# Performance work log

Hardware: AMD Instinct MI355X
Metric: run time of the kernel (lower is better)

The kernel has to match this reference:

```python
import jax, jax.numpy as jnp
import numpy as np

S, B, D, H, F, E = 2048, 8, 512, 8, 2048, 64
CAP_FACTOR = 2
EPS = 1e-5


def setup_inputs() -> dict:
    key = jax.random.key(0)
    ks = jax.random.split(key, 12)
    s = 0.02
    return {
        "src": jax.random.normal(ks[0], (S, B, D), jnp.float32),
        "in_proj_w": jax.random.normal(ks[1], (3 * D, D), jnp.float32) * s,
        "in_proj_b": jnp.zeros((3 * D,), jnp.float32),
        "out_proj_w": jax.random.normal(ks[2], (D, D), jnp.float32) * s,
        "out_proj_b": jnp.zeros((D,), jnp.float32),
        "ln1_g": jnp.ones((D,), jnp.float32),
        "ln1_b": jnp.zeros((D,), jnp.float32),
        "gate_w": jax.random.normal(ks[3], (D, E), jnp.float32) * s,
        "w1": jax.random.normal(ks[4], (E, D, F), jnp.float32) * s,
        "b1": jnp.zeros((E, F), jnp.float32),
        "w2": jax.random.normal(ks[5], (E, F, D), jnp.float32) * s,
        "b2": jnp.zeros((E, D), jnp.float32),
        "ln2_g": jnp.ones((D,), jnp.float32),
        "ln2_b": jnp.zeros((D,), jnp.float32),
    }


def _layer_norm(x, g, b):
    mu = jnp.mean(x, -1, keepdims=True)
    var = jnp.mean(jnp.square(x - mu), -1, keepdims=True)
    return (x - mu) * jax.lax.rsqrt(var + EPS) * g + b


def reference(src, in_proj_w, in_proj_b, out_proj_w, out_proj_b,
              ln1_g, ln1_b, gate_w, w1, b1, w2, b2, ln2_g, ln2_b):
    hd = D // H
    # --- self attention (seq-first, as nn.MultiheadAttention) ---
    qkv = src @ in_proj_w.T + in_proj_b            # [S,B,3D]
    q, k, v = jnp.split(qkv, 3, axis=-1)
    q = q.reshape(S, B, H, hd)
    k = k.reshape(S, B, H, hd)
    v = v.reshape(S, B, H, hd)
    scores = jnp.einsum('qbhd,kbhd->bhqk', q, k) * (hd ** -0.5)
    attn = jax.nn.softmax(scores, axis=-1)
    ctx = jnp.einsum('bhqk,kbhd->qbhd', attn, v).reshape(S, B, D)
    attn_out = ctx @ out_proj_w.T + out_proj_b
    x = _layer_norm(src + attn_out, ln1_g, ln1_b)

    # --- MoE: top-1 gating + capacity dispatch + merged expert FFN ---
    N = S * B
    C = CAP_FACTOR * N // E                         # per-expert capacity
    xt = x.reshape(N, D)
    probs = jax.nn.softmax(xt @ gate_w, axis=-1)    # [N,E]
    eidx = jnp.argmax(probs, axis=-1)               # [N]
    gval = jnp.take_along_axis(probs, eidx[:, None], 1)[:, 0]
    onehot = jax.nn.one_hot(eidx, E, dtype=jnp.int32)
    pos = jnp.take_along_axis(jnp.cumsum(onehot, 0), eidx[:, None], 1)[:, 0] - 1
    pos_s = jnp.where(pos < C, pos, C)              # overflow tokens -> dummy slot C
    buf = jnp.zeros((E, C + 1, D), xt.dtype).at[eidx, pos_s].set(xt)
    xe = buf[:, :C]                                 # [E,C,D]
    h = jax.nn.relu(jnp.einsum('ecd,edf->ecf', xe, w1) + b1[:, None, :])
    ye = jnp.einsum('ecf,efd->ecd', h, w2) + b2[:, None, :]
    ye = jnp.pad(ye, ((0, 0), (0, 1), (0, 0)))      # slot C = zeros (dropped)
    yt = ye[eidx, pos_s] * gval[:, None]            # combine with gate weight
    moe_out = yt.reshape(S, B, D)

    return _layer_norm(x + moe_out, ln2_g, ln2_b)
```

## Files before the change

### kernel.cpp

```cpp
#include <hip/hip_runtime.h>
#include <hip/hip_bf16.h>

typedef __bf16 bf16_t;
typedef __bf16 bf16x8 __attribute__((ext_vector_type(8)));
typedef float f32x4 __attribute__((ext_vector_type(4)));

static constexpr int S_ = 2048;
static constexpr int B_ = 8;
static constexpr int D_ = 512;
static constexpr int H_ = 8;
static constexpr int HD_ = 64;
static constexpr int F_ = 2048;
static constexpr int E_ = 64;
static constexpr int NT = S_ * B_;
static constexpr int CAP = 512;
static constexpr float EPS_ = 1e-5f;

__device__ __forceinline__ float wave_sum(float v) {
#pragma unroll
  for (int m = 1; m < 64; m <<= 1) v += __shfl_xor(v, m);
  return v;
}

__global__ void k_cvt(const float* __restrict__ in, bf16_t* __restrict__ out, int n8) {
  int i = blockIdx.x * blockDim.x + threadIdx.x;
  if (i >= n8) return;
  const float4* p = (const float4*)in + (size_t)i * 2;
  float4 a = p[0], b = p[1];
  bf16x8 o;
  o[0]=(bf16_t)a.x; o[1]=(bf16_t)a.y; o[2]=(bf16_t)a.z; o[3]=(bf16_t)a.w;
  o[4]=(bf16_t)b.x; o[5]=(bf16_t)b.y; o[6]=(bf16_t)b.z; o[7]=(bf16_t)b.w;
  ((bf16x8*)out)[i] = o;
}

__global__ void k_tcvt(const float* __restrict__ in, bf16_t* __restrict__ out,
                       int R, int C, long strideIn, long strideOut) {
  __shared__ __align__(16) float t[64][68];
  const float* ip = in + (long)blockIdx.z * strideIn;
  bf16_t* op = out + (long)blockIdx.z * strideOut;
  int r0 = blockIdx.y * 64, c0 = blockIdx.x * 64;
  int tid = threadIdx.x;
  int row = tid >> 2, cc = (tid & 3) * 16;
  const float4* g = (const float4*)(ip + (long)(r0 + row) * C + c0 + cc);
  float4 a0 = g[0], a1 = g[1], a2 = g[2], a3 = g[3];
  *(float4*)&t[row][cc + 0]  = a0;
  *(float4*)&t[row][cc + 4]  = a1;
  *(float4*)&t[row][cc + 8]  = a2;
  *(float4*)&t[row][cc + 12] = a3;
  __syncthreads();
  int oc = tid >> 2, rr = (tid & 3) * 16;
  bf16x8 o0, o1;
#pragma unroll
  for (int j = 0; j < 8; j++) o0[j] = (bf16_t)t[rr + j][oc];
#pragma unroll
  for (int j = 0; j < 8; j++) o1[j] = (bf16_t)t[rr + 8 + j][oc];
  *(bf16x8*)(op + (long)(c0 + oc) * R + r0 + rr)     = o0;
  *(bf16x8*)(op + (long)(c0 + oc) * R + r0 + rr + 8) = o1;
}

__global__ void k_tv(const bf16_t* __restrict__ qkv, bf16_t* __restrict__ vT) {
  __shared__ __align__(16) bf16_t t[64][72];
  int bh = blockIdx.y, bI = bh >> 3, hI = bh & 7;
  int s0 = blockIdx.x * 64;
  int tid = threadIdx.x;
  int row = tid >> 2, cc = (tid & 3) * 16;
  const uint4* g = (const uint4*)(qkv + ((long)(s0 + row) * B_ + bI) * 1536 + 1024 + hI * 64 + cc);
  uint4 v0 = g[0], v1 = g[1];
  *(uint4*)&t[row][cc]     = v0;
  *(uint4*)&t[row][cc + 8] = v1;
  __syncthreads();
  int oc = tid >> 2, rr = (tid & 3) * 16;
  bf16x8 o0, o1;
#pragma unroll
  for (int j = 0; j < 8; j++) o0[j] = t[rr + j][oc];
#pragma unroll
  for (int j = 0; j < 8; j++) o1[j] = t[rr + 8 + j][oc];
  bf16_t* op = vT + ((long)bh * 64 + oc) * (long)S_ + s0 + rr;
  *(bf16x8*)(op)     = o0;
  *(bf16x8*)(op + 8) = o1;
}

template <int RELU>
__global__ __launch_bounds__(256) void k_gemm(
    const bf16_t* __restrict__ A, const bf16_t* __restrict__ Bm,
    const float* __restrict__ bias, bf16_t* __restrict__ Cout,
    int K, int lda, int ldb, int ldc,
    long aStride, long bStride, long cStride, int biasStride,
    const int* __restrict__ cnt, int mCap) {
  __shared__ __align__(16) bf16_t As[128 * 32];
  __shared__ __align__(16) bf16_t Bs[128 * 32];
  int z = blockIdx.z;
  if (cnt) {
    int c = cnt[z]; if (c > mCap) c = mCap;
    if ((int)blockIdx.y * 128 >= c) return;
  }
  long m0 = (long)blockIdx.y * 128, n0 = (long)blockIdx.x * 128;
  const bf16_t* Ab = A + (long)z * aStride + m0 * lda;
  const bf16_t* Bb = Bm + (long)z * bStride + n0 * ldb;
  int tid = threadIdx.x, wid = tid >> 6, lane = tid & 63;
  int lr = lane & 15, lg = lane >> 4;
  int wm = wid >> 1, wn = wid & 1;
  int srow = tid >> 1, scol = (tid & 1) * 16;
  f32x4 acc[4][4] = {};
  const uint4* ga = (const uint4*)(Ab + (long)srow * lda + scol);
  const uint4* gb = (const uint4*)(Bb + (long)srow * ldb + scol);
  uint4 ra0 = ga[0], ra1 = ga[1], rb0 = gb[0], rb1 = gb[1];
  for (int k0 = 0; k0 < K; k0 += 32) {
    *(uint4*)&As[srow * 32 + scol]     = ra0;
    *(uint4*)&As[srow * 32 + scol + 8] = ra1;
    *(uint4*)&Bs[srow * 32 + scol]     = rb0;
    *(uint4*)&Bs[srow * 32 + scol + 8] = rb1;
    __syncthreads();
    if (k0 + 32 < K) {
      ga = (const uint4*)(Ab + (long)srow * lda + (k0 + 32) + scol);
      gb = (const uint4*)(Bb + (long)srow * ldb + (k0 + 32) + scol);
      ra0 = ga[0]; ra1 = ga[1]; rb0 = gb[0]; rb1 = gb[1];
    }
    bf16x8 af[4], bfr[4];
#pragma unroll
    for (int i = 0; i < 4; i++) {
      af[i]  = *(const bf16x8*)&As[(wm * 64 + i * 16 + lr) * 32 + lg * 8];
      bfr[i] = *(const bf16x8*)&Bs[(wn * 64 + i * 16 + lr) * 32 + lg * 8];
    }
#pragma unroll
    for (int i = 0; i < 4; i++)
#pragma unroll
      for (int j = 0; j < 4; j++)
        acc[i][j] = __builtin_amdgcn_mfma_f32_16x16x32_bf16(af[i], bfr[j], acc[i][j], 0, 0, 0);
    __syncthreads();
  }
#pragma unroll
  for (int j = 0; j < 4; j++) {
    int col = (int)n0 + wn * 64 + j * 16 + lr;
    float bv = bias[(long)z * biasStride + col];
#pragma unroll
    for (int i = 0; i < 4; i++) {
      long row = m0 + wm * 64 + i * 16 + lg * 4;
#pragma unroll
      for (int r = 0; r < 4; r++) {
        float v = acc[i][j][r] + bv;
        if (RELU) v = fmaxf(v, 0.0f);
        Cout[(long)z * cStride + (row + r) * ldc + col] = (bf16_t)v;
      }
    }
  }
}

__global__ __launch_bounds__(256) void k_attn(const bf16_t* __restrict__ qkv,
                                              const bf16_t* __restrict__ vT,
                                              bf16_t* __restrict__ ctx) {
  constexpr int LP = 80;
  __shared__ __align__(16) bf16_t Kld[64 * LP];
  __shared__ __align__(16) bf16_t Vld[64 * LP];
  __shared__ __align__(16) bf16_t Pld[4][16 * LP];
  int bh = blockIdx.y, bI = bh >> 3, hI = bh & 7;
  int q0 = blockIdx.x * 64;
  int tid = threadIdx.x, wid = tid >> 6, lane = tid & 63;
  int lr = lane & 15, lg = lane >> 4;
  int qrow = q0 + wid * 16 + lr;
  const bf16_t* qb = qkv + ((long)qrow * B_ + bI) * 1536 + hI * 64;
  bf16x8 qf0 = *(const bf16x8*)(qb + lg * 8);
  bf16x8 qf1 = *(const bf16x8*)(qb + 32 + lg * 8);
  f32x4 o[4] = {};
  float mrun[4], lrun[4];
#pragma unroll
  for (int r = 0; r < 4; r++) { mrun[r] = -3.0e38f; lrun[r] = 0.0f; }
  int srow = tid >> 2, sc = (tid & 3) * 16;
  for (int kb = 0; kb < S_ / 64; kb++) {
    int krow = kb * 64 + srow;
    const uint4* kg = (const uint4*)(qkv + ((long)krow * B_ + bI) * 1536 + 512 + hI * 64 + sc);
    const uint4* vg = (const uint4*)(vT + ((long)bh * 64 + srow) * (long)S_ + kb * 64 + sc);
    uint4 k0v = kg[0], k1v = kg[1], v0v = vg[0], v1v = vg[1];
    __syncthreads();
    *(uint4*)&Kld[srow * LP + sc]     = k0v;
    *(uint4*)&Kld[srow * LP + sc + 8] = k1v;
    *(uint4*)&Vld[srow * LP + sc]     = v0v;
    *(uint4*)&Vld[srow * LP + sc + 8] = v1v;
    __syncthreads();
    f32x4 sacc[4] = {};
#pragma unroll
    for (int kc = 0; kc < 2; kc++) {
      bf16x8 qf = kc ? qf1 : qf0;
#pragma unroll
      for (int kt = 0; kt < 4; kt++) {
        bf16x8 kf = *(const bf16x8*)&Kld[(kt * 16 + lr) * LP + kc * 32 + lg * 8];
        sacc[kt] = __builtin_amdgcn_mfma_f32_16x16x32_bf16(qf, kf, sacc[kt], 0, 0, 0);
      }
    }
#pragma unroll
    for (int kt = 0; kt < 4; kt++) sacc[kt] *= 0.125f;
    float pv[4][4];
#pragma unroll
    for (int r = 0; r < 4; r++) {
      float mx = fmaxf(fmaxf(sacc[0][r], sacc[1][r]), fmaxf(sacc[2][r], sacc[3][r]));
      mx = fmaxf(mx, __shfl_xor(mx, 1));
      mx = fmaxf(mx, __shfl_xor(mx, 2));
      mx = fmaxf(mx, __shfl_xor(mx, 4));
      mx = fmaxf(mx, __shfl_xor(mx, 8));
      float mnew = fmaxf(mrun[r], mx);
      float corr = __expf(mrun[r] - mnew);
      float ps = 0.0f;
#pragma unroll
      for (int kt = 0; kt < 4; kt++) {
        float p = __expf(sacc[kt][r] - mnew);
        pv[kt][r] = p; ps += p;
      }
      ps += __shfl_xor(ps, 1); ps += __shfl_xor(ps, 2);
      ps += __shfl_xor(ps, 4); ps += __shfl_xor(ps, 8);
      lrun[r] = lrun[r] * corr + ps;
      mrun[r] = mnew;
#pragma unroll
      for (int nt = 0; nt < 4; nt++) o[nt][r] *= corr;
    }
#pragma unroll
    for (int kt = 0; kt < 4; kt++)
#pragma unroll
      for (int r = 0; r < 4; r++)
        Pld[wid][(lg * 4 + r) * LP + kt * 16 + lr] = (bf16_t)pv[kt][r];
#pragma unroll
    for (int ks = 0; ks < 2; ks++) {
      bf16x8 pa = *(const bf16x8*)&Pld[wid][lr * LP + ks * 32 + lg * 8];
#pragma unroll
      for (int nt = 0; nt < 4; nt++) {
        bf16x8 vb = *(const bf16x8*)&Vld[(nt * 16 + lr) * LP + ks * 32 + lg * 8];
        o[nt] = __builtin_amdgcn_mfma_f32_16x16x32_bf16(pa, vb, o[nt], 0, 0, 0);
      }
    }
  }
#pragma unroll
  for (int nt = 0; nt < 4; nt++)
#pragma unroll
    for (int r = 0; r < 4; r++) {
      int qr = q0 + wid * 16 + lg * 4 + r;
      float val = o[nt][r] / lrun[r];
      ctx[((long)qr * B_ + bI) * (long)D_ + hI * 64 + nt * 16 + lr] = (bf16_t)val;
    }
}

__global__ void k_ln_res(const float* __restrict__ base, const bf16_t* __restrict__ addb,
                         const float* __restrict__ g, const float* __restrict__ b,
                         float* __restrict__ out) {
  int w = (int)((blockIdx.x * blockDim.x + threadIdx.x) >> 6);
  int lane = threadIdx.x & 63;
  if (w >= NT) return;
  long off = (long)w * D_ + lane * 8;
  const float4* pb = (const float4*)(base + off);
  float4 b0 = pb[0], b1 = pb[1];
  bf16x8 av = *(const bf16x8*)(addb + off);
  float t[8];
  t[0]=b0.x+(float)av[0]; t[1]=b0.y+(float)av[1]; t[2]=b0.z+(float)av[2]; t[3]=b0.w+(float)av[3];
  t[4]=b1.x+(float)av[4]; t[5]=b1.y+(float)av[5]; t[6]=b1.z+(float)av[6]; t[7]=b1.w+(float)av[7];
  float s = t[0]+t[1]+t[2]+t[3]+t[4]+t[5]+t[6]+t[7];
  s = wave_sum(s);
  float mu = s * (1.0f / D_);
  float vv = 0.0f;
#pragma unroll
  for (int j = 0; j < 8; j++) { float d = t[j] - mu; vv += d * d; }
  vv = wave_sum(vv);
  float rstd = rsqrtf(vv * (1.0f / D_) + EPS_);
  const float4* pg = (const float4*)(g + lane * 8);
  const float4* pq = (const float4*)(b + lane * 8);
  float4 g0 = pg[0], g1 = pg[1], q0 = pq[0], q1 = pq[1];
  float4 o0, o1;
  o0.x=(t[0]-mu)*rstd*g0.x+q0.x; o0.y=(t[1]-mu)*rstd*g0.y+q0.y;
  o0.z=(t[2]-mu)*rstd*g0.z+q0.z; o0.w=(t[3]-mu)*rstd*g0.w+q0.w;
  o1.x=(t[4]-mu)*rstd*g1.x+q1.x; o1.y=(t[5]-mu)*rstd*g1.y+q1.y;
  o1.z=(t[6]-mu)*rstd*g1.z+q1.z; o1.w=(t[7]-mu)*rstd*g1.w+q1.w;
  float4* po = (float4*)(out + off);
  po[0] = o0; po[1] = o1;
}

__global__ void k_gate(const float* __restrict__ x, const float* __restrict__ gw,
                       int* __restrict__ eidx, float* __restrict__ gval) {
  int w = (int)((blockIdx.x * blockDim.x + threadIdx.x) >> 6);
  int lane = threadIdx.x & 63;
  if (w >= NT) return;
  const float* xr = x + (long)w * D_;
  float a0 = 0.0f, a1 = 0.0f, a2 = 0.0f, a3 = 0.0f;
#pragma unroll 4
  for (int k = 0; k < D_; k += 4) {
    a0 = fmaf(xr[k + 0], gw[(k + 0) * E_ + lane], a0);
    a1 = fmaf(xr[k + 1], gw[(k + 1) * E_ + lane], a1);
    a2 = fmaf(xr[k + 2], gw[(k + 2) * E_ + lane], a2);
    a3 = fmaf(xr[k + 3], gw[(k + 3) * E_ + lane], a3);
  }
  float acc = (a0 + a1) + (a2 + a3);
  float v = acc; int idx = lane;
#pragma unroll
  for (int m = 1; m < 64; m <<= 1) {
    float ov = __shfl_xor(v, m);
    int oi = __shfl_xor(idx, m);
    if (ov > v || (ov == v && oi < idx)) { v = ov; idx = oi; }
  }
  float s = __expf(acc - v);
  s = wave_sum(s);
  if (lane == 0) { eidx[w] = idx; gval[w] = 1.0f / s; }
}

__global__ void k_route(const float* __restrict__ x, const int* __restrict__ eidx,
                        int* __restrict__ pos, int* __restrict__ cnt,
                        bf16_t* __restrict__ xe) {
  int w = (int)((blockIdx.x * blockDim.x + threadIdx.x) >> 6);
  int lane = threadIdx.x & 63;
  if (w >= NT) return;
  int e = eidx[w];
  int p = 0;
  if (lane == 0) p = atomicAdd(&cnt[e], 1);
  p = __shfl(p, 0);
  if (lane == 0) pos[w] = p;
  if (p < CAP) {
    const float4* px = (const float4*)(x + (long)w * D_ + lane * 8);
    float4 a = px[0], b = px[1];
    bf16x8 o;
    o[0]=(bf16_t)a.x; o[1]=(bf16_t)a.y; o[2]=(bf16_t)a.z; o[3]=(bf16_t)a.w;
    o[4]=(bf16_t)b.x; o[5]=(bf16_t)b.y; o[6]=(bf16_t)b.z; o[7]=(bf16_t)b.w;
    *(bf16x8*)(xe + ((long)e * CAP + p) * D_ + lane * 8) = o;
  }
}

__global__ void k_final(const float* __restrict__ x, const bf16_t* __restrict__ ye,
                        const int* __restrict__ eidx, const int* __restrict__ pos,
                        const float* __restrict__ gval,
                        const float* __restrict__ g, const float* __restrict__ b,
                        float* __restrict__ out) {
  int w = (int)((blockIdx.x * blockDim.x + threadIdx.x) >> 6);
  int lane = threadIdx.x & 63;
  if (w >= NT) return;
  int e = eidx[w], p = pos[w];
  float gv = gval[w];
  long off = (long)w * D_ + lane * 8;
  const float4* px = (const float4*)(x + off);
  float4 x0 = px[0], x1 = px[1];
  float t[8] = {x0.x, x0.y, x0.z, x0.w, x1.x, x1.y, x1.z, x1.w};
  if (p < CAP) {
    bf16x8 yv = *(const bf16x8*)(ye + ((long)e * CAP + p) * D_ + lane * 8);
#pragma unroll
    for (int j = 0; j < 8; j++) t[j] += (float)yv[j] * gv;
  }
  float s = t[0]+t[1]+t[2]+t[3]+t[4]+t[5]+t[6]+t[7];
  s = wave_sum(s);
  float mu = s * (1.0f / D_);
  float vv = 0.0f;
#pragma unroll
  for (int j = 0; j < 8; j++) { float d = t[j] - mu; vv += d * d; }
  vv = wave_sum(vv);
  float rstd = rsqrtf(vv * (1.0f / D_) + EPS_);
  const float4* pg = (const float4*)(g + lane * 8);
  const float4* pq = (const float4*)(b + lane * 8);
  float4 g0 = pg[0], g1 = pg[1], q0 = pq[0], q1 = pq[1];
  float4 o0, o1;
  o0.x=(t[0]-mu)*rstd*g0.x+q0.x; o0.y=(t[1]-mu)*rstd*g0.y+q0.y;
  o0.z=(t[2]-mu)*rstd*g0.z+q0.z; o0.w=(t[3]-mu)*rstd*g0.w+q0.w;
  o1.x=(t[4]-mu)*rstd*g1.x+q1.x; o1.y=(t[5]-mu)*rstd*g1.y+q1.y;
  o1.z=(t[6]-mu)*rstd*g1.z+q1.z; o1.w=(t[7]-mu)*rstd*g1.w+q1.w;
  float4* po = (float4*)(out + off);
  po[0] = o0; po[1] = o1;
}

extern "C" void kernel_launch(void* const* d_in, const int* in_sizes, int n_in,
                              void* d_out, int out_size, void* d_ws, size_t ws_size,
                              hipStream_t stream) {
  const float* src        = (const float*)d_in[0];
  const float* in_proj_w  = (const float*)d_in[1];
  const float* in_proj_b  = (const float*)d_in[2];
  const float* out_proj_w = (const float*)d_in[3];
  const float* out_proj_b = (const float*)d_in[4];
  const float* ln1_g      = (const float*)d_in[5];
  const float* ln1_b      = (const float*)d_in[6];
  const float* gate_w     = (const float*)d_in[7];
  const float* w1         = (const float*)d_in[8];
  const float* b1         = (const float*)d_in[9];
  const float* w2         = (const float*)d_in[10];
  const float* b2         = (const float*)d_in[11];
  const float* ln2_g      = (const float*)d_in[12];
  const float* ln2_b      = (const float*)d_in[13];
  (void)in_sizes; (void)n_in; (void)out_size; (void)ws_size;

  char* ws = (char*)d_ws;
  size_t off = 0;
  auto alloc = [&](size_t bytes) -> char* {
    char* p = ws + off; off += (bytes + 255) & ~(size_t)255; return p;
  };
  bf16_t* src_bf  = (bf16_t*)alloc((size_t)NT * D_ * 2);
  bf16_t* w_in_bf = (bf16_t*)alloc((size_t)3 * D_ * D_ * 2);
  bf16_t* w_out_bf= (bf16_t*)alloc((size_t)D_ * D_ * 2);
  bf16_t* qkv_bf  = (bf16_t*)alloc((size_t)NT * 3 * D_ * 2);
  bf16_t* vT      = (bf16_t*)alloc((size_t)B_ * H_ * HD_ * S_ * 2);
  bf16_t* ctx_bf  = (bf16_t*)alloc((size_t)NT * D_ * 2);
  bf16_t* ao_bf   = (bf16_t*)alloc((size_t)NT * D_ * 2);
  float*  x_f32   = (float*)alloc((size_t)NT * D_ * 4);
  bf16_t* w1t     = (bf16_t*)alloc((size_t)E_ * D_ * F_ * 2);
  bf16_t* w2t     = (bf16_t*)alloc((size_t)E_ * F_ * D_ * 2);
  bf16_t* xe      = (bf16_t*)alloc((size_t)E_ * CAP * D_ * 2);
  bf16_t* hbuf    = (bf16_t*)alloc((size_t)E_ * CAP * F_ * 2);
  bf16_t* ye      = (bf16_t*)alloc((size_t)E_ * CAP * D_ * 2);
  int*    eidx    = (int*)alloc((size_t)NT * 4);
  int*    pos     = (int*)alloc((size_t)NT * 4);
  float*  gval    = (float*)alloc((size_t)NT * 4);
  int*    cnt     = (int*)alloc((size_t)E_ * 4);

  k_cvt<<<NT * D_ / 8 / 256, 256, 0, stream>>>(src, src_bf, NT * D_ / 8);
  k_cvt<<<3 * D_ * D_ / 8 / 256, 256, 0, stream>>>(in_proj_w, w_in_bf, 3 * D_ * D_ / 8);
  k_cvt<<<D_ * D_ / 8 / 256, 256, 0, stream>>>(out_proj_w, w_out_bf, D_ * D_ / 8);
  k_tcvt<<<dim3(F_ / 64, D_ / 64, E_), 256, 0, stream>>>(w1, w1t, D_, F_, (long)D_ * F_, (long)D_ * F_);
  k_tcvt<<<dim3(D_ / 64, F_ / 64, E_), 256, 0, stream>>>(w2, w2t, F_, D_, (long)F_ * D_, (long)F_ * D_);

  k_gemm<0><<<dim3(12, 128, 1), 256, 0, stream>>>(src_bf, w_in_bf, in_proj_b, qkv_bf,
      512, 512, 512, 1536, 0, 0, 0, 0, nullptr, NT);

  k_tv<<<dim3(S_ / 64, B_ * H_), 256, 0, stream>>>(qkv_bf, vT);
  k_attn<<<dim3(S_ / 64, B_ * H_), 256, 0, stream>>>(qkv_bf, vT, ctx_bf);
  k_gemm<0><<<dim3(4, 128, 1), 256, 0, stream>>>(ctx_bf, w_out_bf, out_proj_b, ao_bf,
      512, 512, 512, 512, 0, 0, 0, 0, nullptr, NT);
  k_ln_res<<<NT / 4, 256, 0, stream>>>(src, ao_bf, ln1_g, ln1_b, x_f32);

  k_gate<<<NT / 4, 256, 0, stream>>>(x_f32, gate_w, eidx, gval);
  hipMemsetAsync(cnt, 0, E_ * 4, stream);
  hipMemsetAsync(xe, 0, (size_t)E_ * CAP * D_ * 2, stream);
  k_route<<<NT / 4, 256, 0, stream>>>(x_f32, eidx, pos, cnt, xe);

  k_gemm<1><<<dim3(F_ / 128, CAP / 128, E_), 256, 0, stream>>>(xe, w1t, b1, hbuf,
      512, 512, 512, 2048, (long)CAP * D_, (long)F_ * D_, (long)CAP * F_, F_, cnt, CAP);
  k_gemm<0><<<dim3(D_ / 128, CAP / 128, E_), 256, 0, stream>>>(hbuf, w2t, b2, ye,
      2048, 2048, 2048, 512, (long)CAP * F_, (long)F_ * D_, (long)CAP * D_, D_, cnt, CAP);

  k_final<<<NT / 4, 256, 0, stream>>>(x_f32, ye, eidx, pos, gval, ln2_g, ln2_b, (float*)d_out);
}
```

Measured before the change: 1.379 ms.

## Use direct global-to-LDS loads in GEMM and lazy rescaling exp2 softmax in attention

```diff
diff --git a/kernel.cpp b/kernel.cpp
--- a/kernel.cpp
+++ b/kernel.cpp
@@ -20,6 +20,11 @@
 #pragma unroll
   for (int m = 1; m < 64; m <<= 1) v += __shfl_xor(v, m);
   return v;
+}
+
+__device__ __forceinline__ void gload_lds16(const void* g, void* l) {
+  __builtin_amdgcn_global_load_lds((const __attribute__((address_space(1))) void*)g,
+                                   (__attribute__((address_space(3))) void*)l, 16, 0, 0);
 }
 
 __global__ void k_cvt(const float* __restrict__ in, bf16_t* __restrict__ out, int n8) {
@@ -100,22 +105,23 @@
   int tid = threadIdx.x, wid = tid >> 6, lane = tid & 63;
   int lr = lane & 15, lg = lane >> 4;
   int wm = wid >> 1, wn = wid & 1;
-  int srow = tid >> 1, scol = (tid & 1) * 16;
+  int grow = wid * 16 + (lane >> 2);
+  int gcol = (lane & 3) * 8;
+  const bf16_t* gA0 = Ab + (long)grow * lda + gcol;
+  const bf16_t* gA1 = gA0 + (long)64 * lda;
+  const bf16_t* gB0 = Bb + (long)grow * ldb + gcol;
+  const bf16_t* gB1 = gB0 + (long)64 * ldb;
+  bf16_t* lA0 = &As[wid * 512 + lane * 8];
+  bf16_t* lA1 = lA0 + 2048;
+  bf16_t* lB0 = &Bs[wid * 512 + lane * 8];
+  bf16_t* lB1 = lB0 + 2048;
   f32x4 acc[4][4] = {};
-  const uint4* ga = (const uint4*)(Ab + (long)srow * lda + scol);
-  const uint4* gb = (const uint4*)(Bb + (long)srow * ldb + scol);
-  uint4 ra0 = ga[0], ra1 = ga[1], rb0 = gb[0], rb1 = gb[1];
   for (int k0 = 0; k0 < K; k0 += 32) {
-    *(uint4*)&As[srow * 32 + scol]     = ra0;
-    *(uint4*)&As[srow * 32 + scol + 8] = ra1;
-    *(uint4*)&Bs[srow * 32 + scol]     = rb0;
-    *(uint4*)&Bs[srow * 32 + scol + 8] = rb1;
+    gload_lds16(gA0 + k0, lA0);
+    gload_lds16(gA1 + k0, lA1);
+    gload_lds16(gB0 + k0, lB0);
+    gload_lds16(gB1 + k0, lB1);
     __syncthreads();
-    if (k0 + 32 < K) {
-      ga = (const uint4*)(Ab + (long)srow * lda + (k0 + 32) + scol);
-      gb = (const uint4*)(Bb + (long)srow * ldb + (k0 + 32) + scol);
-      ra0 = ga[0]; ra1 = ga[1]; rb0 = gb[0]; rb1 = gb[1];
-    }
     bf16x8 af[4], bfr[4];
 #pragma unroll
     for (int i = 0; i < 4; i++) {
@@ -149,7 +155,7 @@
 __global__ __launch_bounds__(256) void k_attn(const bf16_t* __restrict__ qkv,
                                               const bf16_t* __restrict__ vT,
                                               bf16_t* __restrict__ ctx) {
-  constexpr int LP = 80;
+  constexpr int LP = 72;
   __shared__ __align__(16) bf16_t Kld[64 * LP];
   __shared__ __align__(16) bf16_t Vld[64 * LP];
   __shared__ __align__(16) bf16_t Pld[4][16 * LP];
@@ -165,6 +171,7 @@
   float mrun[4], lrun[4];
 #pragma unroll
   for (int r = 0; r < 4; r++) { mrun[r] = -3.0e38f; lrun[r] = 0.0f; }
+  const float SC = 0.125f * 1.44269504f;
   int srow = tid >> 2, sc = (tid & 3) * 16;
   for (int kb = 0; kb < S_ / 64; kb++) {
     int krow = kb * 64 + srow;
@@ -188,7 +195,7 @@
       }
     }
 #pragma unroll
-    for (int kt = 0; kt < 4; kt++) sacc[kt] *= 0.125f;
+    for (int kt = 0; kt < 4; kt++) sacc[kt] *= SC;
     float pv[4][4];
 #pragma unroll
     for (int r = 0; r < 4; r++) {
@@ -197,20 +204,23 @@
       mx = fmaxf(mx, __shfl_xor(mx, 2));
       mx = fmaxf(mx, __shfl_xor(mx, 4));
       mx = fmaxf(mx, __shfl_xor(mx, 8));
-      float mnew = fmaxf(mrun[r], mx);
-      float corr = __expf(mrun[r] - mnew);
+      if (__any(mx > mrun[r] + 8.0f)) {
+        float mnew = fmaxf(mrun[r], mx);
+        float corr = exp2f(mrun[r] - mnew);
+        lrun[r] *= corr;
+#pragma unroll
+        for (int nt = 0; nt < 4; nt++) o[nt][r] *= corr;
+        mrun[r] = mnew;
+      }
       float ps = 0.0f;
 #pragma unroll
       for (int kt = 0; kt < 4; kt++) {
-        float p = __expf(sacc[kt][r] - mnew);
+        float p = exp2f(sacc[kt][r] - mrun[r]);
         pv[kt][r] = p; ps += p;
       }
       ps += __shfl_xor(ps, 1); ps += __shfl_xor(ps, 2);
       ps += __shfl_xor(ps, 4); ps += __shfl_xor(ps, 8);
-      lrun[r] = lrun[r] * corr + ps;
-      mrun[r] = mnew;
-#pragma unroll
-      for (int nt = 0; nt < 4; nt++) o[nt][r] *= corr;
+      lrun[r] += ps;
     }
 #pragma unroll
     for (int kt = 0; kt < 4; kt++)
```

Result: slower. 1.421 ms (+3.1%).
